# Performance work log

Measured on AMD Instinct MI355X. Metric: run time of the kernel, lower is better.

Reference implementation:

```python
import jax, jax.numpy as jnp
import numpy as np

RES_MIN, RES_MAX, L, S_DIM = 16, 256, 16, 512
T = 65536           # hash table entries per level (power of 2)
B = 8
N = RES_MAX * RES_MAX
PRIME = np.uint32(2654435761)


def _res_levels():
    # Instant-NGP geometric progression of grid resolutions.
    b = (RES_MAX / RES_MIN) ** (1.0 / (L - 1))
    r = np.round(RES_MIN * b ** np.arange(L)).astype(np.int64)
    return np.minimum(r, RES_MAX)

RES_LEVELS = _res_levels()


def _sample_coords():
    # row-major grid, coord = (x, y) normalized to (0,1), index n = y*R + x
    yy, xx = np.meshgrid(np.arange(RES_MAX), np.arange(RES_MAX), indexing='ij')
    c = np.stack([(xx + 0.5) / RES_MAX, (yy + 0.5) / RES_MAX], axis=-1)
    return c.reshape(-1, 2).astype(np.float32)  # [N, 2]


def hash_retrieve(tables, coords):
    # tables: [B, L, T, 2], coords: [N, 2] in (0,1) -> [B, N, L*2]
    res_f = jnp.asarray(RES_LEVELS, jnp.float32)[:, None, None]          # [L,1,1]
    pos = coords[None, :, :] * (res_f - 1.0)                              # [L,N,2]
    pos0 = jnp.floor(pos)
    frac = pos - pos0                                                     # [L,N,2]
    i0 = pos0.astype(jnp.uint32)
    imax = (jnp.asarray(RES_LEVELS, jnp.uint32) - 1)[:, None, None]
    i1 = jnp.minimum(i0 + 1, imax)
    x0, y0 = i0[..., 0], i0[..., 1]
    x1, y1 = i1[..., 0], i1[..., 1]

    def hsh(xi, yi):  # spatial hash mod table size
        return ((xi ^ (yi * PRIME)) % np.uint32(T)).astype(jnp.int32)

    idx = jnp.stack([hsh(x0, y0), hsh(x1, y0), hsh(x0, y1), hsh(x1, y1)], -1)  # [L,N,4]
    tab = jnp.transpose(tables, (1, 0, 2, 3))                             # [L,B,T,2]
    # per-level gather: [L,B,N,4,2]
    g = jax.vmap(lambda t, i: t[:, i], in_axes=(0, 0))(tab, idx)
    fx, fy = frac[..., 0], frac[..., 1]
    w = jnp.stack([(1 - fx) * (1 - fy), fx * (1 - fy), (1 - fx) * fy, fx * fy], -1)  # [L,N,4]
    feats = jnp.sum(g * w[:, None, :, :, None], axis=3)                   # [L,B,N,2]
    feats = jnp.transpose(feats, (1, 2, 0, 3))                            # [B,N,L,2]
    return feats.reshape(feats.shape[0], feats.shape[1], L * 2)


def mod_linear(xin, s, w, aw, ab, bias, activ):
    # StyleGAN2 modulated linear with demodulation.
    style = s @ aw.T + ab                                 # [B, in]
    wmod = w[None, :, :] * style[:, None, :]              # [B, out, in]
    demod = jax.lax.rsqrt(jnp.sum(wmod * wmod, -1) + 1e-8)  # [B, out]
    y = jnp.einsum('bni,boi->bno', xin, wmod) * demod[:, None, :] + bias
    return activ(y)


def setup_inputs() -> dict:
    key = jax.random.key(0)
    ks = jax.random.split(key, 16)
    d = {
        'x': jax.random.normal(ks[0], (B, L, T * 2), jnp.float32),
        's': jax.random.normal(ks[1], (B, S_DIM), jnp.float32),
        'coords': jnp.asarray(_sample_coords()),
    }
    dims = [(L * 2, 32), (32, 32), (32, 3)]
    for i, (cin, cout) in enumerate(dims):
        d[f'w{i}'] = jax.random.normal(ks[2 + 4 * i], (cout, cin), jnp.float32) / np.sqrt(cin)
        d[f'aw{i}'] = jax.random.normal(ks[3 + 4 * i], (cin, S_DIM), jnp.float32) / np.sqrt(S_DIM)
        d[f'ab{i}'] = jnp.ones((cin,), jnp.float32)
        d[f'b{i}'] = jnp.zeros((cout,), jnp.float32)
    return d


def reference(x, s, coords, w0, aw0, ab0, b0, w1, aw1, ab1, b1, w2, aw2, ab2, b2):
    tables = x.reshape(B, L, T, 2)
    h = hash_retrieve(tables, coords)                      # [B, N, 32]
    h = mod_linear(h, s, w0, aw0, ab0, b0, jax.nn.relu)
    h = mod_linear(h, s, w1, aw1, ab1, b1, jax.nn.relu)
    h = mod_linear(h, s, w2, aw2, ab2, b2, jnp.tanh)       # [B, N, 3]
    img = h.reshape(B, RES_MAX, RES_MAX, 3)
    return jnp.transpose(img, (0, 3, 1, 2))                # [B,3,H,W]
```

## Files before the change

kernel.cpp:

```cpp
#include <hip/hip_runtime.h>
#include <math.h>

#define LVL 16
#define TBL 65536
#define BATCH 8
#define NPIX 65536
#define SDIM 512
#define HPRIME 2654435761u

typedef __attribute__((ext_vector_type(2))) float f32x2;

struct ResPack { int r[LVL]; };
struct OffPack { int o[LVL]; };

#define WEFF_STRIDE 2144
#define STYLE_OFF   17152
#define GRIDS_OFF   17920

__global__ __launch_bounds__(256) void style_kernel(
    const float* __restrict__ s,
    const float* __restrict__ aw0, const float* __restrict__ ab0,
    const float* __restrict__ aw1, const float* __restrict__ ab1,
    const float* __restrict__ aw2, const float* __restrict__ ab2,
    float* __restrict__ ws)
{
    const int wave_id = blockIdx.x * 4 + ((int)threadIdx.x >> 6);
    const int lane    = (int)threadIdx.x & 63;
    const int b = wave_id / 96;
    const int v = wave_id % 96;

    const float* row; float bias;
    if (v < 32)      { row = aw0 + v * SDIM;        bias = ab0[v]; }
    else if (v < 64) { row = aw1 + (v - 32) * SDIM; bias = ab1[v - 32]; }
    else             { row = aw2 + (v - 64) * SDIM; bias = ab2[v - 64]; }

    const float* sb = s + b * SDIM;
    float acc = 0.f;
    #pragma unroll
    for (int j = 0; j < SDIM / 64; ++j) {
        const int k = lane + j * 64;
        acc += sb[k] * row[k];
    }
    #pragma unroll
    for (int off = 32; off >= 1; off >>= 1) acc += __shfl_xor(acc, off, 64);
    if (lane == 0) ws[STYLE_OFF + b * 96 + v] = acc + bias;
}

__global__ __launch_bounds__(256) void weff_kernel(
    const float* __restrict__ w0, const float* __restrict__ w1, const float* __restrict__ w2,
    float* __restrict__ ws)
{
    const int b = blockIdx.x;
    __shared__ float st[96];
    __shared__ float demod[67];
    const int tid = (int)threadIdx.x;

    if (tid < 96) st[tid] = ws[STYLE_OFF + b * 96 + tid];
    __syncthreads();

    if (tid < 67) {
        const int o = tid;
        const float* wrow; const float* stp;
        if (o < 32)      { wrow = w0 + o * 32;        stp = st; }
        else if (o < 64) { wrow = w1 + (o - 32) * 32; stp = st + 32; }
        else             { wrow = w2 + (o - 64) * 32; stp = st + 64; }
        float sum = 0.f;
        #pragma unroll
        for (int i = 0; i < 32; ++i) { float v = wrow[i] * stp[i]; sum += v * v; }
        demod[o] = 1.0f / sqrtf(sum + 1e-8f);
    }
    __syncthreads();

    float* outp = ws + b * WEFF_STRIDE;
    for (int idx = tid; idx < 2144; idx += 256) {
        float v;
        if (idx < 1024) {
            const int o2 = idx >> 6, rem = idx & 63, i = rem >> 1, h = rem & 1;
            const int o = o2 + 16 * h;
            v = w0[o * 32 + i] * st[i] * demod[o];
        } else if (idx < 2048) {
            const int j = idx - 1024;
            const int o2 = j >> 6, rem = j & 63, i = rem >> 1, h = rem & 1;
            const int o = o2 + 16 * h;
            v = w1[o * 32 + i] * st[32 + i] * demod[32 + o];
        } else {
            const int j = idx - 2048; const int o = j >> 5, i = j & 31;
            v = w2[j] * st[64 + i] * demod[64 + o];
        }
        outp[idx] = v;
    }
}

__global__ __launch_bounds__(256) void grid_kernel(
    const float* __restrict__ tables,
    float2* __restrict__ grids,
    int grid_tot, ResPack res, OffPack off)
{
    const int bid = (int)blockIdx.x;
    const int b = bid & 7;
    const int l = (bid >> 3) & 15;
    const int chunk = bid >> 7;
    const int R = res.r[l];
    const int idx = chunk * 256 + (int)threadIdx.x;
    if (idx >= R * R) return;
    const int y = idx / R;
    const int x = idx - y * R;
    const unsigned h = ((unsigned)x ^ ((unsigned)y * HPRIME)) & 0xFFFFu;
    const float2* tl = (const float2*)(tables + ((size_t)b * LVL + l) * (TBL * 2));
    grids[(size_t)b * grid_tot + off.o[l] + idx] = tl[h];
}

__global__ __launch_bounds__(256) void fused_kernel(
    const float2* __restrict__ grids,
    const float* __restrict__ coords,
    const float* __restrict__ weff,
    const float* __restrict__ b0, const float* __restrict__ b1, const float* __restrict__ b2,
    float* __restrict__ out,
    int grid_tot, ResPack res, OffPack off)
{
    const int b     = blockIdx.x & 7;
    const int chunk = blockIdx.x >> 3;
    const int n     = chunk * 256 + (int)threadIdx.x;

    const float cx = coords[2 * n];
    const float cy = coords[2 * n + 1];
    const float2* gb = grids + (size_t)b * grid_tot;

    float feat[32];
    #pragma unroll
    for (int l = 0; l < LVL; ++l) {
        const int R = res.r[l];
        const float rm1 = (float)(R - 1);
        const float px = cx * rm1, py = cy * rm1;
        const float fpx = floorf(px), fpy = floorf(py);
        const float fx = px - fpx, fy = py - fpy;
        int x0 = (int)fpx, y0 = (int)fpy;
        int x1 = x0 + 1; if (x1 > R - 1) x1 = R - 1;
        int y1 = y0 + 1; if (y1 > R - 1) y1 = R - 1;
        const float2* gl = gb + off.o[l];
        const int ry0 = y0 * R, ry1 = y1 * R;
        const float2 g00 = gl[ry0 + x0];
        const float2 g10 = gl[ry0 + x1];
        const float2 g01 = gl[ry1 + x0];
        const float2 g11 = gl[ry1 + x1];
        const float w00 = (1.f - fx) * (1.f - fy);
        const float w10 = fx * (1.f - fy);
        const float w01 = (1.f - fx) * fy;
        const float w11 = fx * fy;
        feat[2 * l]     = g00.x * w00 + g10.x * w10 + g01.x * w01 + g11.x * w11;
        feat[2 * l + 1] = g00.y * w00 + g10.y * w10 + g01.y * w01 + g11.y * w11;
    }

    const f32x2* W0p = (const f32x2*)(weff + (size_t)b * WEFF_STRIDE);
    const f32x2* W1p = W0p + 512;
    const float* W2  = weff + (size_t)b * WEFF_STRIDE + 2048;

    f32x2 h1p[16];
    #pragma unroll
    for (int o2 = 0; o2 < 16; ++o2) {
        f32x2 acc; acc[0] = b0[o2]; acc[1] = b0[o2 + 16];
        #pragma unroll
        for (int i = 0; i < 32; ++i) {
            f32x2 fb; fb[0] = feat[i]; fb[1] = feat[i];
            acc += W0p[o2 * 32 + i] * fb;
        }
        acc[0] = fmaxf(acc[0], 0.f); acc[1] = fmaxf(acc[1], 0.f);
        h1p[o2] = acc;
    }

    f32x2 h2p[16];
    #pragma unroll
    for (int o2 = 0; o2 < 16; ++o2) {
        f32x2 acc; acc[0] = b1[o2]; acc[1] = b1[o2 + 16];
        #pragma unroll
        for (int i = 0; i < 32; ++i) {
            const float hv = h1p[i & 15][i >> 4];
            f32x2 fb; fb[0] = hv; fb[1] = hv;
            acc += W1p[o2 * 32 + i] * fb;
        }
        acc[0] = fmaxf(acc[0], 0.f); acc[1] = fmaxf(acc[1], 0.f);
        h2p[o2] = acc;
    }

    #pragma unroll
    for (int o = 0; o < 3; ++o) {
        float acc = b2[o];
        #pragma unroll
        for (int i = 0; i < 32; ++i)
            acc = fmaf(W2[o * 32 + i], h2p[i & 15][i >> 4], acc);
        out[((size_t)(b * 3 + o) << 16) + n] = tanhf(acc);
    }
}

__global__ __launch_bounds__(256) void fused_direct(
    const float* __restrict__ tables, const float* __restrict__ coords,
    const float* __restrict__ weff,
    const float* __restrict__ b0, const float* __restrict__ b1, const float* __restrict__ b2,
    float* __restrict__ out, ResPack res)
{
    const int b     = blockIdx.x & 7;
    const int chunk = blockIdx.x >> 3;
    const int n     = chunk * 256 + (int)threadIdx.x;
    const float cx = coords[2 * n];
    const float cy = coords[2 * n + 1];
    const float* tb = tables + (size_t)b * (LVL * TBL * 2);

    float feat[32];
    #pragma unroll
    for (int l = 0; l < LVL; ++l) {
        const int R = res.r[l];
        const float rm1 = (float)(R - 1);
        const float px = cx * rm1, py = cy * rm1;
        const float fpx = floorf(px), fpy = floorf(py);
        const float fx = px - fpx, fy = py - fpy;
        unsigned x0 = (unsigned)fpx, y0 = (unsigned)fpy;
        const unsigned im = (unsigned)(R - 1);
        unsigned x1 = x0 + 1u; if (x1 > im) x1 = im;
        unsigned y1 = y0 + 1u; if (y1 > im) y1 = im;
        const unsigned hy0 = y0 * HPRIME, hy1 = y1 * HPRIME;
        const unsigned h00 = (x0 ^ hy0) & 0xFFFFu;
        const unsigned h10 = (x1 ^ hy0) & 0xFFFFu;
        const unsigned h01 = (x0 ^ hy1) & 0xFFFFu;
        const unsigned h11 = (x1 ^ hy1) & 0xFFFFu;
        const float2* tl = (const float2*)(tb + l * (TBL * 2));
        const float2 g00 = tl[h00];
        const float2 g10 = tl[h10];
        const float2 g01 = tl[h01];
        const float2 g11 = tl[h11];
        const float w00 = (1.f - fx) * (1.f - fy);
        const float w10 = fx * (1.f - fy);
        const float w01 = (1.f - fx) * fy;
        const float w11 = fx * fy;
        feat[2 * l]     = g00.x * w00 + g10.x * w10 + g01.x * w01 + g11.x * w11;
        feat[2 * l + 1] = g00.y * w00 + g10.y * w10 + g01.y * w01 + g11.y * w11;
    }

    const f32x2* W0p = (const f32x2*)(weff + (size_t)b * WEFF_STRIDE);
    const f32x2* W1p = W0p + 512;
    const float* W2  = weff + (size_t)b * WEFF_STRIDE + 2048;

    f32x2 h1p[16];
    #pragma unroll
    for (int o2 = 0; o2 < 16; ++o2) {
        f32x2 acc; acc[0] = b0[o2]; acc[1] = b0[o2 + 16];
        #pragma unroll
        for (int i = 0; i < 32; ++i) {
            f32x2 fb; fb[0] = feat[i]; fb[1] = feat[i];
            acc += W0p[o2 * 32 + i] * fb;
        }
        acc[0] = fmaxf(acc[0], 0.f); acc[1] = fmaxf(acc[1], 0.f);
        h1p[o2] = acc;
    }
    f32x2 h2p[16];
    #pragma unroll
    for (int o2 = 0; o2 < 16; ++o2) {
        f32x2 acc; acc[0] = b1[o2]; acc[1] = b1[o2 + 16];
        #pragma unroll
        for (int i = 0; i < 32; ++i) {
            const float hv = h1p[i & 15][i >> 4];
            f32x2 fb; fb[0] = hv; fb[1] = hv;
            acc += W1p[o2 * 32 + i] * fb;
        }
        acc[0] = fmaxf(acc[0], 0.f); acc[1] = fmaxf(acc[1], 0.f);
        h2p[o2] = acc;
    }
    #pragma unroll
    for (int o = 0; o < 3; ++o) {
        float acc = b2[o];
        #pragma unroll
        for (int i = 0; i < 32; ++i)
            acc = fmaf(W2[o * 32 + i], h2p[i & 15][i >> 4], acc);
        out[((size_t)(b * 3 + o) << 16) + n] = tanhf(acc);
    }
}

extern "C" void kernel_launch(void* const* d_in, const int* in_sizes, int n_in,
                              void* d_out, int out_size, void* d_ws, size_t ws_size,
                              hipStream_t stream) {
    const float* x      = (const float*)d_in[0];
    const float* s      = (const float*)d_in[1];
    const float* coords = (const float*)d_in[2];
    const float* w0  = (const float*)d_in[3];
    const float* aw0 = (const float*)d_in[4];
    const float* ab0 = (const float*)d_in[5];
    const float* b0  = (const float*)d_in[6];
    const float* w1  = (const float*)d_in[7];
    const float* aw1 = (const float*)d_in[8];
    const float* ab1 = (const float*)d_in[9];
    const float* b1  = (const float*)d_in[10];
    const float* w2  = (const float*)d_in[11];
    const float* aw2 = (const float*)d_in[12];
    const float* ab2 = (const float*)d_in[13];
    const float* b2  = (const float*)d_in[14];
    float* out = (float*)d_out;
    float* ws  = (float*)d_ws;

    ResPack rp; OffPack op;
    int grid_tot = 0;
    const double g = pow(256.0 / 16.0, 1.0 / 15.0);
    for (int l = 0; l < LVL; ++l) {
        double r = 16.0 * pow(g, (double)l);
        long ri = lround(r);
        if (ri > 256) ri = 256;
        rp.r[l] = (int)ri;
        op.o[l] = grid_tot;
        grid_tot += (int)(ri * ri);
    }

    const size_t need = (size_t)GRIDS_OFF * 4 + (size_t)grid_tot * 8 * BATCH;

    hipLaunchKernelGGL(style_kernel, dim3(192), dim3(256), 0, stream,
                       s, aw0, ab0, aw1, ab1, aw2, ab2, ws);
    hipLaunchKernelGGL(weff_kernel, dim3(BATCH), dim3(256), 0, stream,
                       w0, w1, w2, ws);

    if (ws_size >= need) {
        float2* grids = (float2*)(ws + GRIDS_OFF);
        hipLaunchKernelGGL(grid_kernel, dim3(BATCH * LVL * (TBL / 256)), dim3(256), 0, stream,
                           x, grids, grid_tot, rp, op);
        hipLaunchKernelGGL(fused_kernel, dim3(NPIX / 256 * BATCH), dim3(256), 0, stream,
                           grids, coords, ws, b0, b1, b2, out, grid_tot, rp, op);
    } else {
        hipLaunchKernelGGL(fused_direct, dim3(NPIX / 256 * BATCH), dim3(256), 0, stream,
                           x, coords, ws, b0, b1, b2, out, rp);
    }
}
```

Before: 175.9 us.

## Gather finest level directly from hash table and compact grid precompute launch

The finest level (256x256) is no longer precomputed into the dense grid buffer. The fused kernel now hashes and gathers it straight from the table, so that large grid is never written and then re-read. The grid kernel launches only as many blocks as the remaining levels need, using per-level block offsets, instead of a fixed 256 blocks per level, most of which exited early. It replaces the integer divide with a float-reciprocal row computation and drops the x1/y1 clamps, which assumes coords lie strictly inside (0,1); the last level's gathers become random hash accesses.

```diff
diff --git a/kernel.cpp b/kernel.cpp
--- a/kernel.cpp
+++ b/kernel.cpp
@@ -12,6 +12,8 @@
 
 struct ResPack { int r[LVL]; };
 struct OffPack { int o[LVL]; };
+struct BlkPack { int o[LVL]; };
+struct RcpPack { float f[LVL]; };
 
 #define WEFF_STRIDE 2144
 #define STYLE_OFF   17152
@@ -94,16 +96,22 @@
 __global__ __launch_bounds__(256) void grid_kernel(
     const float* __restrict__ tables,
     float2* __restrict__ grids,
-    int grid_tot, ResPack res, OffPack off)
-{
-    const int bid = (int)blockIdx.x;
-    const int b = bid & 7;
-    const int l = (bid >> 3) & 15;
-    const int chunk = bid >> 7;
+    int grid_tot, int bpb,
+    ResPack res, OffPack off, BlkPack blk, RcpPack rcp)
+{
+    const int bid  = (int)blockIdx.x;
+    const int b    = bid / bpb;
+    const int lblk = bid - b * bpb;
+
+    int l = 0;
+    #pragma unroll
+    for (int k = 1; k < 15; ++k) l += (lblk >= blk.o[k]) ? 1 : 0;
+
     const int R = res.r[l];
-    const int idx = chunk * 256 + (int)threadIdx.x;
+    const int idx = (lblk - blk.o[l]) * 256 + (int)threadIdx.x;
     if (idx >= R * R) return;
-    const int y = idx / R;
+
+    const int y = (int)(((float)idx + 0.5f) * rcp.f[l]);
     const int x = idx - y * R;
     const unsigned h = ((unsigned)x ^ ((unsigned)y * HPRIME)) & 0xFFFFu;
     const float2* tl = (const float2*)(tables + ((size_t)b * LVL + l) * (TBL * 2));
@@ -111,6 +119,7 @@
 }
 
 __global__ __launch_bounds__(256) void fused_kernel(
+    const float* __restrict__ tables,
     const float2* __restrict__ grids,
     const float* __restrict__ coords,
     const float* __restrict__ weff,
@@ -126,34 +135,62 @@
     const float cy = coords[2 * n + 1];
     const float2* gb = grids + (size_t)b * grid_tot;
 
-    float feat[32];
-    #pragma unroll
-    for (int l = 0; l < LVL; ++l) {
+    f32x2 feat2[16];
+
+    #pragma unroll
+    for (int l = 0; l < 15; ++l) {
         const int R = res.r[l];
         const float rm1 = (float)(R - 1);
         const float px = cx * rm1, py = cy * rm1;
         const float fpx = floorf(px), fpy = floorf(py);
         const float fx = px - fpx, fy = py - fpy;
-        int x0 = (int)fpx, y0 = (int)fpy;
-        int x1 = x0 + 1; if (x1 > R - 1) x1 = R - 1;
-        int y1 = y0 + 1; if (y1 > R - 1) y1 = R - 1;
+        const int x0 = (int)fpx, y0 = (int)fpy;
         const float2* gl = gb + off.o[l];
-        const int ry0 = y0 * R, ry1 = y1 * R;
-        const float2 g00 = gl[ry0 + x0];
-        const float2 g10 = gl[ry0 + x1];
-        const float2 g01 = gl[ry1 + x0];
-        const float2 g11 = gl[ry1 + x1];
+        const int base = y0 * R + x0;
+        const float2 g00 = gl[base];
+        const float2 g10 = gl[base + 1];
+        const float2 g01 = gl[base + R];
+        const float2 g11 = gl[base + R + 1];
         const float w00 = (1.f - fx) * (1.f - fy);
         const float w10 = fx * (1.f - fy);
         const float w01 = (1.f - fx) * fy;
         const float w11 = fx * fy;
-        feat[2 * l]     = g00.x * w00 + g10.x * w10 + g01.x * w01 + g11.x * w11;
-        feat[2 * l + 1] = g00.y * w00 + g10.y * w10 + g01.y * w01 + g11.y * w11;
+        f32x2 acc;
+        acc[0] = g00.x * w00; acc[1] = g00.y * w00;
+        acc[0] += g10.x * w10; acc[1] += g10.y * w10;
+        acc[0] += g01.x * w01; acc[1] += g01.y * w01;
+        acc[0] += g11.x * w11; acc[1] += g11.y * w11;
+        feat2[l] = acc;
+    }
+    {
+        const float rm1 = 255.f;
+        const float px = cx * rm1, py = cy * rm1;
+        const float fpx = floorf(px), fpy = floorf(py);
+        const float fx = px - fpx, fy = py - fpy;
+        const unsigned x0 = (unsigned)(int)fpx, y0 = (unsigned)(int)fpy;
+        const unsigned hy0 = (y0 * HPRIME) & 0xFFFFu;
+        const unsigned hy1 = ((y0 + 1u) * HPRIME) & 0xFFFFu;
+        const float2* tl = (const float2*)(tables + ((size_t)b * LVL + 15) * (TBL * 2));
+        const float2 g00 = tl[(x0 ^ hy0) & 0xFFFFu];
+        const float2 g10 = tl[((x0 + 1u) ^ hy0) & 0xFFFFu];
+        const float2 g01 = tl[(x0 ^ hy1) & 0xFFFFu];
+        const float2 g11 = tl[((x0 + 1u) ^ hy1) & 0xFFFFu];
+        const float w00 = (1.f - fx) * (1.f - fy);
+        const float w10 = fx * (1.f - fy);
+        const float w01 = (1.f - fx) * fy;
+        const float w11 = fx * fy;
+        f32x2 acc;
+        acc[0] = g00.x * w00; acc[1] = g00.y * w00;
+        acc[0] += g10.x * w10; acc[1] += g10.y * w10;
+        acc[0] += g01.x * w01; acc[1] += g01.y * w01;
+        acc[0] += g11.x * w11; acc[1] += g11.y * w11;
+        feat2[15] = acc;
     }
 
     const f32x2* W0p = (const f32x2*)(weff + (size_t)b * WEFF_STRIDE);
     const f32x2* W1p = W0p + 512;
     const float* W2  = weff + (size_t)b * WEFF_STRIDE + 2048;
+    const float* featf = (const float*)feat2;
 
     f32x2 h1p[16];
     #pragma unroll
@@ -161,7 +198,7 @@
         f32x2 acc; acc[0] = b0[o2]; acc[1] = b0[o2 + 16];
         #pragma unroll
         for (int i = 0; i < 32; ++i) {
-            f32x2 fb; fb[0] = feat[i]; fb[1] = feat[i];
+            f32x2 fb; fb[0] = featf[i]; fb[1] = featf[i];
             acc += W0p[o2 * 32 + i] * fb;
         }
         acc[0] = fmaxf(acc[0], 0.f); acc[1] = fmaxf(acc[1], 0.f);
@@ -214,14 +251,11 @@
         const float fpx = floorf(px), fpy = floorf(py);
         const float fx = px - fpx, fy = py - fpy;
         unsigned x0 = (unsigned)fpx, y0 = (unsigned)fpy;
-        const unsigned im = (unsigned)(R - 1);
-        unsigned x1 = x0 + 1u; if (x1 > im) x1 = im;
-        unsigned y1 = y0 + 1u; if (y1 > im) y1 = im;
-        const unsigned hy0 = y0 * HPRIME, hy1 = y1 * HPRIME;
+        const unsigned hy0 = (y0 * HPRIME), hy1 = ((y0 + 1u) * HPRIME);
         const unsigned h00 = (x0 ^ hy0) & 0xFFFFu;
-        const unsigned h10 = (x1 ^ hy0) & 0xFFFFu;
+        const unsigned h10 = ((x0 + 1u) ^ hy0) & 0xFFFFu;
         const unsigned h01 = (x0 ^ hy1) & 0xFFFFu;
-        const unsigned h11 = (x1 ^ hy1) & 0xFFFFu;
+        const unsigned h11 = ((x0 + 1u) ^ hy1) & 0xFFFFu;
         const float2* tl = (const float2*)(tb + l * (TBL * 2));
         const float2 g00 = tl[h00];
         const float2 g10 = tl[h10];
@@ -295,16 +329,21 @@
     float* out = (float*)d_out;
     float* ws  = (float*)d_ws;
 
-    ResPack rp; OffPack op;
-    int grid_tot = 0;
+    ResPack rp; OffPack op; BlkPack bp; RcpPack cp;
+    int grid_tot = 0, bpb = 0;
     const double g = pow(256.0 / 16.0, 1.0 / 15.0);
     for (int l = 0; l < LVL; ++l) {
         double r = 16.0 * pow(g, (double)l);
         long ri = lround(r);
         if (ri > 256) ri = 256;
         rp.r[l] = (int)ri;
+        cp.f[l] = 1.0f / (float)ri;
         op.o[l] = grid_tot;
-        grid_tot += (int)(ri * ri);
+        bp.o[l] = bpb;
+        if (l < 15) {
+            grid_tot += (int)(ri * ri);
+            bpb += (int)((ri * ri + 255) / 256);
+        }
     }
 
     const size_t need = (size_t)GRIDS_OFF * 4 + (size_t)grid_tot * 8 * BATCH;
@@ -316,10 +355,10 @@
 
     if (ws_size >= need) {
         float2* grids = (float2*)(ws + GRIDS_OFF);
-        hipLaunchKernelGGL(grid_kernel, dim3(BATCH * LVL * (TBL / 256)), dim3(256), 0, stream,
-                           x, grids, grid_tot, rp, op);
+        hipLaunchKernelGGL(grid_kernel, dim3(BATCH * bpb), dim3(256), 0, stream,
+                           x, grids, grid_tot, bpb, rp, op, bp, cp);
         hipLaunchKernelGGL(fused_kernel, dim3(NPIX / 256 * BATCH), dim3(256), 0, stream,
-                           grids, coords, ws, b0, b1, b2, out, grid_tot, rp, op);
+                           x, grids, coords, ws, b0, b1, b2, out, grid_tot, rp, op);
     } else {
         hipLaunchKernelGGL(fused_direct, dim3(NPIX / 256 * BATCH), dim3(256), 0, stream,
                            x, coords, ws, b0, b1, b2, out, rp);
```

Measured after the change: 171.5 us. 2.5% less time.
